# Kernel optimization log

Measured on AMD Instinct MI355X. Metric: run time of the kernel, lower is better.

Reference implementation:

```python
import jax, jax.numpy as jnp
import numpy as np

D = 1024  # input_size
NORM = 1.0 / np.sqrt(D)


def setup_inputs() -> dict:
    key = jax.random.key(0)
    k_x, k_q, k_k, k_v = jax.random.split(key, 4)
    B, S = 4, 2048
    scale = 1.0 / np.sqrt(D)  # init ~ nn.Linear default magnitude
    return {
        "inputs": jax.random.normal(k_x, (B, S, D), dtype=jnp.float32),
        "Wq": jax.random.uniform(k_q, (D, D), jnp.float32, -scale, scale),
        "Wk": jax.random.uniform(k_k, (D, D), jnp.float32, -scale, scale),
        "Wv": jax.random.uniform(k_v, (D, D), jnp.float32, -scale, scale),
    }


def reference(inputs, Wq, Wk, Wv):
    # nn.Linear(x) = x @ W.T (no bias)
    Q = jnp.einsum("bsd,ed->bse", inputs, Wq)
    K = jnp.einsum("bsd,ed->bse", inputs, Wk)
    V = jnp.einsum("bsd,ed->bse", inputs, Wv)
    attn = jnp.einsum("bqe,bke->bqk", Q, K) * NORM  # [B,S,S]
    attn = jax.nn.softmax(attn, axis=2)
    return jnp.einsum("bqk,bke->bqe", attn, V)
```

## Files before the change

kernel.cpp:

```cpp
#include <hip/hip_runtime.h>

typedef __bf16 bf16_t;
typedef __bf16 bf16x8 __attribute__((ext_vector_type(8)));
typedef __bf16 bf16x4 __attribute__((ext_vector_type(4)));
typedef float  floatx4 __attribute__((ext_vector_type(4)));

__device__ __forceinline__ void gload_lds16(const bf16_t* g, bf16_t* l) {
    __builtin_amdgcn_global_load_lds(
        (const __attribute__((address_space(1))) void*)g,
        (__attribute__((address_space(3))) void*)l,
        16, 0, 0);
}

template <int MODE, int BKT, typename OutT>
__global__ __launch_bounds__(256) void gemm_nt(
    const bf16_t* __restrict__ A, int lda, size_t batchA,
    const bf16_t* __restrict__ B, int ldb, size_t batchB,
    OutT* __restrict__ C, int ldc, size_t batchC,
    bf16_t* __restrict__ C2, int ldc2,
    float* __restrict__ rowsums, int batchR,
    int K, float scale)
{
    constexpr int CH  = BKT / 8;
    constexpr int RPS = 2048 / BKT;
    constexpr int NSHOT = 128 / RPS;

    __shared__ bf16_t sA[128 * BKT];
    __shared__ bf16_t sB[128 * BKT];

    A += (size_t)blockIdx.z * batchA;
    B += (size_t)blockIdx.z * batchB;

    const int tid  = threadIdx.x;
    const int wid  = tid >> 6;
    const int lane = tid & 63;

    const int bm = blockIdx.x * 128;
    const int bn = blockIdx.y * 128;

    const int rr  = tid / CH;
    const int kc8 = (((tid & (CH - 1)) ^ (rr & (CH - 1))) << 3);

    const int wy = (wid >> 1) * 64;
    const int wx = (wid & 1) * 64;
    const int lr = lane & 15;

    floatx4 acc[4][4] = {};

    const bf16_t* pa = A + (size_t)(bm + rr) * lda + kc8;
    const bf16_t* pb = B + (size_t)(bn + rr) * ldb + kc8;
    bf16_t* la = &sA[wid * 512];
    bf16_t* lb = &sB[wid * 512];

    for (int k0 = 0; k0 < K; k0 += BKT) {
        #pragma unroll
        for (int c = 0; c < NSHOT; ++c) {
            gload_lds16(pa + (size_t)(c * RPS) * lda + k0, la + c * 2048);
            gload_lds16(pb + (size_t)(c * RPS) * ldb + k0, lb + c * 2048);
        }
        __syncthreads();

        #pragma unroll
        for (int kk = 0; kk < BKT / 32; ++kk) {
            const int cch = (kk << 2) + (lane >> 4);
            bf16x8 af[4], bq[4];
            #pragma unroll
            for (int i = 0; i < 4; ++i) {
                int r = wy + i * 16 + lr;
                af[i] = *(const bf16x8*)&sA[r * BKT + ((cch ^ (r & (CH - 1))) << 3)];
            }
            #pragma unroll
            for (int j = 0; j < 4; ++j) {
                int r = wx + j * 16 + lr;
                bq[j] = *(const bf16x8*)&sB[r * BKT + ((cch ^ (r & (CH - 1))) << 3)];
            }
            #pragma unroll
            for (int i = 0; i < 4; ++i)
                #pragma unroll
                for (int j = 0; j < 4; ++j)
                    acc[i][j] = __builtin_amdgcn_mfma_f32_16x16x32_bf16(
                        bq[j], af[i], acc[i][j], 0, 0, 0);
        }
        __syncthreads();
    }

    const int cfix = lane & 15;
    const int creg = (lane >> 4) << 2;

    if constexpr (MODE == 1) {
        if (blockIdx.z == 2) {
            #pragma unroll
            for (int i = 0; i < 4; ++i) {
                int mg = bm + wy + i * 16 + cfix;
                #pragma unroll
                for (int j = 0; j < 4; ++j) {
                    int ng = bn + wx + j * 16 + creg;
                    #pragma unroll
                    for (int r = 0; r < 4; ++r)
                        C2[(size_t)(ng + r) * ldc2 + mg] = (bf16_t)acc[i][j][r];
                }
            }
            return;
        }
        OutT* Cz = C + (size_t)blockIdx.z * batchC;
        #pragma unroll
        for (int i = 0; i < 4; ++i) {
            size_t row = (size_t)(bm + wy + i * 16 + cfix);
            #pragma unroll
            for (int j = 0; j < 4; ++j) {
                int col = bn + wx + j * 16 + creg;
                bf16x4 v;
                #pragma unroll
                for (int r = 0; r < 4; ++r) v[r] = (bf16_t)acc[i][j][r];
                *(bf16x4*)&Cz[row * (size_t)ldc + col] = v;
            }
        }
    } else if constexpr (MODE == 2) {
        OutT* Cz = C + (size_t)blockIdx.z * batchC;
        float* sums = rowsums + (size_t)blockIdx.z * batchR;
        float rs[4] = {0.f, 0.f, 0.f, 0.f};
        #pragma unroll
        for (int i = 0; i < 4; ++i) {
            size_t row = (size_t)(bm + wy + i * 16 + cfix);
            #pragma unroll
            for (int j = 0; j < 4; ++j) {
                int col = bn + wx + j * 16 + creg;
                bf16x4 v;
                #pragma unroll
                for (int r = 0; r < 4; ++r) {
                    v[r] = (bf16_t)__expf(acc[i][j][r] * scale);
                    rs[i] += (float)v[r];
                }
                *(bf16x4*)&Cz[row * (size_t)ldc + col] = v;
            }
        }
        #pragma unroll
        for (int i = 0; i < 4; ++i) {
            rs[i] += __shfl_xor(rs[i], 16);
            rs[i] += __shfl_xor(rs[i], 32);
        }
        if (lane < 16) {
            #pragma unroll
            for (int i = 0; i < 4; ++i)
                atomicAdd(&sums[bm + wy + i * 16 + lane], rs[i]);
        }
    } else {
        OutT* Cz = C + (size_t)blockIdx.z * batchC;
        const float* sums = rowsums + (size_t)blockIdx.z * batchR;
        #pragma unroll
        for (int i = 0; i < 4; ++i) {
            int rloc = bm + wy + i * 16 + cfix;
            float rinv = 1.0f / sums[rloc];
            size_t row = (size_t)rloc;
            #pragma unroll
            for (int j = 0; j < 4; ++j) {
                int col = bn + wx + j * 16 + creg;
                floatx4 v;
                #pragma unroll
                for (int r = 0; r < 4; ++r) v[r] = acc[i][j][r] * rinv;
                *(floatx4*)&Cz[row * (size_t)ldc + col] = v;
            }
        }
    }
}

__global__ __launch_bounds__(256) void cvt_all(
    const float* __restrict__ X, const float* __restrict__ Wq,
    const float* __restrict__ Wk, const float* __restrict__ Wv,
    bf16_t* __restrict__ Xb, bf16_t* __restrict__ Wqb,
    bf16_t* __restrict__ Wkb, bf16_t* __restrict__ Wvb,
    int nX4, int nW4)
{
    int i = blockIdx.x * blockDim.x + threadIdx.x;
    const float* src; bf16_t* dst; int idx;
    if (i < nX4) { src = X; dst = Xb; idx = i; }
    else {
        int j = i - nX4;
        int w = j / nW4;
        idx = j - w * nW4;
        if (i >= nX4 + 3 * nW4) return;
        src = (w == 0) ? Wq : (w == 1) ? Wk : Wv;
        dst = (w == 0) ? Wqb : (w == 1) ? Wkb : Wvb;
    }
    float4 v = ((const float4*)src)[idx];
    bf16x4 o;
    o[0] = (bf16_t)v.x; o[1] = (bf16_t)v.y; o[2] = (bf16_t)v.z; o[3] = (bf16_t)v.w;
    *(bf16x4*)(dst + (size_t)idx * 4) = o;
}

extern "C" void kernel_launch(void* const* d_in, const int* in_sizes, int n_in,
                              void* d_out, int out_size, void* d_ws, size_t ws_size,
                              hipStream_t stream)
{
    (void)in_sizes; (void)n_in; (void)out_size; (void)ws_size;
    const float* X  = (const float*)d_in[0];
    const float* Wq = (const float*)d_in[1];
    const float* Wk = (const float*)d_in[2];
    const float* Wv = (const float*)d_in[3];
    float* out = (float*)d_out;

    const int Bb = 4, S = 2048, D = 1024;
    const int M = Bb * S;

    char* ws = (char*)d_ws;
    size_t off = 0;
    auto carve = [&](size_t bytes) -> char* {
        char* p = ws + off;
        off += (bytes + 255) & ~(size_t)255;
        return p;
    };
    bf16_t* Xb  = (bf16_t*)carve((size_t)M * D * 2);
    bf16_t* Wqb = (bf16_t*)carve((size_t)D * D * 2);
    bf16_t* Wkb = (bf16_t*)carve((size_t)D * D * 2);
    bf16_t* Wvb = (bf16_t*)carve((size_t)D * D * 2);
    bf16_t* Qb  = (bf16_t*)carve((size_t)M * D * 2);
    bf16_t* Kb  = (bf16_t*)carve((size_t)M * D * 2);
    bf16_t* Vt  = (bf16_t*)carve((size_t)D * M * 2);
    bf16_t* Sc  = (bf16_t*)carve((size_t)Bb * S * S * 2);
    float*  sums = (float*)carve((size_t)M * 4);

    hipMemsetAsync(sums, 0, (size_t)M * 4, stream);

    const int nX4 = M * D / 4, nW4 = D * D / 4;
    const int tot4 = nX4 + 3 * nW4;
    cvt_all<<<(tot4 + 255) / 256, 256, 0, stream>>>(
        X, Wq, Wk, Wv, Xb, Wqb, Wkb, Wvb, nX4, nW4);

    gemm_nt<1, 64, bf16_t><<<dim3(M / 128, D / 128, 3), 256, 0, stream>>>(
        Xb, D, 0, Wqb, D, (size_t)D * D, Qb, D, (size_t)M * D,
        Vt, M, nullptr, 0, D, 1.0f);

    gemm_nt<2, 64, bf16_t><<<dim3(S / 128, S / 128, Bb), 256, 0, stream>>>(
        Qb, D, (size_t)S * D, Kb, D, (size_t)S * D, Sc, S, (size_t)S * S,
        nullptr, 0, sums, S, D, 0.03125f);

    gemm_nt<3, 128, float><<<dim3(S / 128, D / 128, Bb), 256, 0, stream>>>(
        Sc, S, (size_t)S * S, Vt, M, (size_t)S, out, D, (size_t)S * D,
        nullptr, 0, sums, S, S, 1.0f);
}
```

Baseline: 242.9 us.

## Fuse conversion and three GEMM stages into one persistent kernel with grid barriers

Replaces the memset, conversion kernel and three separate GEMM launches with a single persistent 512-block kernel. Stages are separated by atomic-counter grid barriers, and the row-sum zeroing moves into the kernel. The aim is to remove launch overhead and inter-kernel gaps. The cost is a fixed grid of 512 blocks, which reduces parallelism for the QK stage (two tiles per block) and the PV stage, and makes correctness depend on every block being co-resident, with a risk of deadlock if they are not. The PV stage also drops from a 128-wide K tile to 64.

Measured after the change: 407.0 us. 1.68x slower.

```diff
diff --git a/kernel.cpp b/kernel.cpp
--- a/kernel.cpp
+++ b/kernel.cpp
@@ -4,6 +4,21 @@
 typedef __bf16 bf16x8 __attribute__((ext_vector_type(8)));
 typedef __bf16 bf16x4 __attribute__((ext_vector_type(4)));
 typedef float  floatx4 __attribute__((ext_vector_type(4)));
+
+#define BK 64
+#define GRID 512
+#define NTHR 256
+
+__device__ __forceinline__ void grid_barrier(unsigned int* cnt, unsigned int target) {
+    __syncthreads();
+    if (threadIdx.x == 0) {
+        __threadfence();
+        atomicAdd(cnt, 1u);
+        while (atomicAdd(cnt, 0u) < target) __builtin_amdgcn_s_sleep(2);
+        __threadfence();
+    }
+    __syncthreads();
+}
 
 __device__ __forceinline__ void gload_lds16(const bf16_t* g, bf16_t* l) {
     __builtin_amdgcn_global_load_lds(
@@ -12,34 +27,21 @@
         16, 0, 0);
 }
 
-template <int MODE, int BKT, typename OutT>
-__global__ __launch_bounds__(256) void gemm_nt(
-    const bf16_t* __restrict__ A, int lda, size_t batchA,
-    const bf16_t* __restrict__ B, int ldb, size_t batchB,
-    OutT* __restrict__ C, int ldc, size_t batchC,
-    bf16_t* __restrict__ C2, int ldc2,
-    float* __restrict__ rowsums, int batchR,
-    int K, float scale)
+template <int MODE>
+__device__ __forceinline__ void gemm_tile(
+    const bf16_t* __restrict__ A, int lda,
+    const bf16_t* __restrict__ B, int ldb,
+    void* __restrict__ Cv, int ldc,
+    float* __restrict__ sums,
+    int bm, int bn, int K, float scale,
+    bf16_t* sA, bf16_t* sB)
 {
-    constexpr int CH  = BKT / 8;
-    constexpr int RPS = 2048 / BKT;
-    constexpr int NSHOT = 128 / RPS;
-
-    __shared__ bf16_t sA[128 * BKT];
-    __shared__ bf16_t sB[128 * BKT];
-
-    A += (size_t)blockIdx.z * batchA;
-    B += (size_t)blockIdx.z * batchB;
-
     const int tid  = threadIdx.x;
     const int wid  = tid >> 6;
     const int lane = tid & 63;
 
-    const int bm = blockIdx.x * 128;
-    const int bn = blockIdx.y * 128;
-
-    const int rr  = tid / CH;
-    const int kc8 = (((tid & (CH - 1)) ^ (rr & (CH - 1))) << 3);
+    const int rr  = tid >> 3;
+    const int kc8 = (((tid & 7) ^ (rr & 7)) << 3);
 
     const int wy = (wid >> 1) * 64;
     const int wx = (wid & 1) * 64;
@@ -52,27 +54,27 @@
     bf16_t* la = &sA[wid * 512];
     bf16_t* lb = &sB[wid * 512];
 
-    for (int k0 = 0; k0 < K; k0 += BKT) {
-        #pragma unroll
-        for (int c = 0; c < NSHOT; ++c) {
-            gload_lds16(pa + (size_t)(c * RPS) * lda + k0, la + c * 2048);
-            gload_lds16(pb + (size_t)(c * RPS) * ldb + k0, lb + c * 2048);
+    for (int k0 = 0; k0 < K; k0 += BK) {
+        #pragma unroll
+        for (int c = 0; c < 4; ++c) {
+            gload_lds16(pa + (size_t)(c * 32) * lda + k0, la + c * 2048);
+            gload_lds16(pb + (size_t)(c * 32) * ldb + k0, lb + c * 2048);
         }
         __syncthreads();
 
         #pragma unroll
-        for (int kk = 0; kk < BKT / 32; ++kk) {
+        for (int kk = 0; kk < 2; ++kk) {
             const int cch = (kk << 2) + (lane >> 4);
             bf16x8 af[4], bq[4];
             #pragma unroll
             for (int i = 0; i < 4; ++i) {
                 int r = wy + i * 16 + lr;
-                af[i] = *(const bf16x8*)&sA[r * BKT + ((cch ^ (r & (CH - 1))) << 3)];
+                af[i] = *(const bf16x8*)&sA[(r << 6) + ((cch ^ (r & 7)) << 3)];
             }
             #pragma unroll
             for (int j = 0; j < 4; ++j) {
                 int r = wx + j * 16 + lr;
-                bq[j] = *(const bf16x8*)&sB[r * BKT + ((cch ^ (r & (CH - 1))) << 3)];
+                bq[j] = *(const bf16x8*)&sB[(r << 6) + ((cch ^ (r & 7)) << 3)];
             }
             #pragma unroll
             for (int i = 0; i < 4; ++i)
@@ -87,51 +89,47 @@
     const int cfix = lane & 15;
     const int creg = (lane >> 4) << 2;
 
-    if constexpr (MODE == 1) {
-        if (blockIdx.z == 2) {
-            #pragma unroll
-            for (int i = 0; i < 4; ++i) {
-                int mg = bm + wy + i * 16 + cfix;
-                #pragma unroll
-                for (int j = 0; j < 4; ++j) {
-                    int ng = bn + wx + j * 16 + creg;
-                    #pragma unroll
-                    for (int r = 0; r < 4; ++r)
-                        C2[(size_t)(ng + r) * ldc2 + mg] = (bf16_t)acc[i][j][r];
-                }
-            }
-            return;
-        }
-        OutT* Cz = C + (size_t)blockIdx.z * batchC;
+    if constexpr (MODE == 0) {
+        bf16_t* C = (bf16_t*)Cv;
         #pragma unroll
         for (int i = 0; i < 4; ++i) {
             size_t row = (size_t)(bm + wy + i * 16 + cfix);
             #pragma unroll
             for (int j = 0; j < 4; ++j) {
-                int col = bn + wx + j * 16 + creg;
                 bf16x4 v;
                 #pragma unroll
                 for (int r = 0; r < 4; ++r) v[r] = (bf16_t)acc[i][j][r];
-                *(bf16x4*)&Cz[row * (size_t)ldc + col] = v;
+                *(bf16x4*)&C[row * (size_t)ldc + (bn + wx + j * 16 + creg)] = v;
+            }
+        }
+    } else if constexpr (MODE == 4) {
+        bf16_t* C = (bf16_t*)Cv;
+        #pragma unroll
+        for (int i = 0; i < 4; ++i) {
+            int mg = bm + wy + i * 16 + cfix;
+            #pragma unroll
+            for (int j = 0; j < 4; ++j) {
+                int ng = bn + wx + j * 16 + creg;
+                #pragma unroll
+                for (int r = 0; r < 4; ++r)
+                    C[(size_t)(ng + r) * ldc + mg] = (bf16_t)acc[i][j][r];
             }
         }
     } else if constexpr (MODE == 2) {
-        OutT* Cz = C + (size_t)blockIdx.z * batchC;
-        float* sums = rowsums + (size_t)blockIdx.z * batchR;
+        bf16_t* C = (bf16_t*)Cv;
         float rs[4] = {0.f, 0.f, 0.f, 0.f};
         #pragma unroll
         for (int i = 0; i < 4; ++i) {
             size_t row = (size_t)(bm + wy + i * 16 + cfix);
             #pragma unroll
             for (int j = 0; j < 4; ++j) {
-                int col = bn + wx + j * 16 + creg;
                 bf16x4 v;
                 #pragma unroll
                 for (int r = 0; r < 4; ++r) {
                     v[r] = (bf16_t)__expf(acc[i][j][r] * scale);
                     rs[i] += (float)v[r];
                 }
-                *(bf16x4*)&Cz[row * (size_t)ldc + col] = v;
+                *(bf16x4*)&C[row * (size_t)ldc + (bn + wx + j * 16 + creg)] = v;
             }
         }
         #pragma unroll
@@ -145,47 +143,95 @@
                 atomicAdd(&sums[bm + wy + i * 16 + lane], rs[i]);
         }
     } else {
-        OutT* Cz = C + (size_t)blockIdx.z * batchC;
-        const float* sums = rowsums + (size_t)blockIdx.z * batchR;
+        float* C = (float*)Cv;
         #pragma unroll
         for (int i = 0; i < 4; ++i) {
             int rloc = bm + wy + i * 16 + cfix;
             float rinv = 1.0f / sums[rloc];
-            size_t row = (size_t)rloc;
-            #pragma unroll
-            for (int j = 0; j < 4; ++j) {
-                int col = bn + wx + j * 16 + creg;
+            #pragma unroll
+            for (int j = 0; j < 4; ++j) {
                 floatx4 v;
                 #pragma unroll
                 for (int r = 0; r < 4; ++r) v[r] = acc[i][j][r] * rinv;
-                *(floatx4*)&Cz[row * (size_t)ldc + col] = v;
-            }
-        }
-    }
-}
-
-__global__ __launch_bounds__(256) void cvt_all(
-    const float* __restrict__ X, const float* __restrict__ Wq,
-    const float* __restrict__ Wk, const float* __restrict__ Wv,
-    bf16_t* __restrict__ Xb, bf16_t* __restrict__ Wqb,
-    bf16_t* __restrict__ Wkb, bf16_t* __restrict__ Wvb,
-    int nX4, int nW4)
+                *(floatx4*)&C[(size_t)rloc * ldc + (bn + wx + j * 16 + creg)] = v;
+            }
+        }
+    }
+}
+
+struct Params {
+    const float *X, *Wq, *Wk, *Wv;
+    bf16_t *Xb, *Wqb, *Wkb, *Wvb, *Qb, *Kb, *Vt, *Sc;
+    float* sums;
+    float* out;
+    unsigned int* cnt;
+};
+
+__global__ __launch_bounds__(NTHR, 2) void attn_mega(Params p)
 {
-    int i = blockIdx.x * blockDim.x + threadIdx.x;
-    const float* src; bf16_t* dst; int idx;
-    if (i < nX4) { src = X; dst = Xb; idx = i; }
-    else {
-        int j = i - nX4;
-        int w = j / nW4;
-        idx = j - w * nW4;
-        if (i >= nX4 + 3 * nW4) return;
-        src = (w == 0) ? Wq : (w == 1) ? Wk : Wv;
-        dst = (w == 0) ? Wqb : (w == 1) ? Wkb : Wvb;
-    }
-    float4 v = ((const float4*)src)[idx];
-    bf16x4 o;
-    o[0] = (bf16_t)v.x; o[1] = (bf16_t)v.y; o[2] = (bf16_t)v.z; o[3] = (bf16_t)v.w;
-    *(bf16x4*)(dst + (size_t)idx * 4) = o;
+    constexpr int S = 2048, D = 1024, M = 8192;
+    constexpr int nX4 = M * D / 4;
+    constexpr int nW4 = D * D / 4;
+    constexpr int tot4 = nX4 + 3 * nW4;
+
+    __shared__ bf16_t sA[128 * BK];
+    __shared__ bf16_t sB[128 * BK];
+
+    const int tid = threadIdx.x;
+    const int blk = blockIdx.x;
+
+    for (int i = blk * NTHR + tid; i < tot4; i += GRID * NTHR) {
+        const float* src; bf16_t* dst; int idx;
+        if (i < nX4) { src = p.X; dst = p.Xb; idx = i; }
+        else {
+            int j = i - nX4;
+            int w = j >> 18;
+            idx = j & (nW4 - 1);
+            src = (w == 0) ? p.Wq : (w == 1) ? p.Wk : p.Wv;
+            dst = (w == 0) ? p.Wqb : (w == 1) ? p.Wkb : p.Wvb;
+        }
+        float4 v = ((const float4*)src)[idx];
+        bf16x4 o;
+        o[0] = (bf16_t)v.x; o[1] = (bf16_t)v.y; o[2] = (bf16_t)v.z; o[3] = (bf16_t)v.w;
+        *(bf16x4*)(dst + (size_t)idx * 4) = o;
+    }
+    {
+        int gi = blk * NTHR + tid;
+        if (gi < M) p.sums[gi] = 0.f;
+    }
+    grid_barrier(p.cnt, GRID);
+
+    {
+        const int bm = (blk & 63) * 128;
+        const int bn = (blk >> 6) * 128;
+        gemm_tile<0>(p.Xb, D, p.Wqb, D, p.Qb, D, nullptr, bm, bn, D, 1.0f, sA, sB);
+        gemm_tile<0>(p.Xb, D, p.Wkb, D, p.Kb, D, nullptr, bm, bn, D, 1.0f, sA, sB);
+        gemm_tile<4>(p.Xb, D, p.Wvb, D, p.Vt, M, nullptr, bm, bn, D, 1.0f, sA, sB);
+    }
+    grid_barrier(p.cnt, 2 * GRID);
+
+    #pragma unroll
+    for (int half = 0; half < 2; ++half) {
+        int t = blk + half * GRID;
+        int z   = t >> 8;
+        int rem = t & 255;
+        int bm = (rem & 15) * 128, bn = (rem >> 4) * 128;
+        gemm_tile<2>(p.Qb + (size_t)z * S * D, D,
+                     p.Kb + (size_t)z * S * D, D,
+                     p.Sc + (size_t)z * S * S, S,
+                     p.sums + z * S, bm, bn, D, 0.03125f, sA, sB);
+    }
+    grid_barrier(p.cnt, 3 * GRID);
+
+    {
+        int z   = blk >> 7;
+        int rem = blk & 127;
+        int bm = (rem & 15) * 128, bn = (rem >> 4) * 128;
+        gemm_tile<3>(p.Sc + (size_t)z * S * S, S,
+                     p.Vt + (size_t)z * S, M,
+                     p.out + (size_t)z * S * D, D,
+                     p.sums + z * S, bm, bn, S, 1.0f, sA, sB);
+    }
 }
 
 extern "C" void kernel_launch(void* const* d_in, const int* in_sizes, int n_in,
@@ -193,48 +239,35 @@
                               hipStream_t stream)
 {
     (void)in_sizes; (void)n_in; (void)out_size; (void)ws_size;
-    const float* X  = (const float*)d_in[0];
-    const float* Wq = (const float*)d_in[1];
-    const float* Wk = (const float*)d_in[2];
-    const float* Wv = (const float*)d_in[3];
-    float* out = (float*)d_out;
-
     const int Bb = 4, S = 2048, D = 1024;
     const int M = Bb * S;
 
     char* ws = (char*)d_ws;
     size_t off = 0;
     auto carve = [&](size_t bytes) -> char* {
-        char* p = ws + off;
+        char* pp = ws + off;
         off += (bytes + 255) & ~(size_t)255;
-        return p;
+        return pp;
     };
-    bf16_t* Xb  = (bf16_t*)carve((size_t)M * D * 2);
-    bf16_t* Wqb = (bf16_t*)carve((size_t)D * D * 2);
-    bf16_t* Wkb = (bf16_t*)carve((size_t)D * D * 2);
-    bf16_t* Wvb = (bf16_t*)carve((size_t)D * D * 2);
-    bf16_t* Qb  = (bf16_t*)carve((size_t)M * D * 2);
-    bf16_t* Kb  = (bf16_t*)carve((size_t)M * D * 2);
-    bf16_t* Vt  = (bf16_t*)carve((size_t)D * M * 2);
-    bf16_t* Sc  = (bf16_t*)carve((size_t)Bb * S * S * 2);
-    float*  sums = (float*)carve((size_t)M * 4);
-
-    hipMemsetAsync(sums, 0, (size_t)M * 4, stream);
-
-    const int nX4 = M * D / 4, nW4 = D * D / 4;
-    const int tot4 = nX4 + 3 * nW4;
-    cvt_all<<<(tot4 + 255) / 256, 256, 0, stream>>>(
-        X, Wq, Wk, Wv, Xb, Wqb, Wkb, Wvb, nX4, nW4);
-
-    gemm_nt<1, 64, bf16_t><<<dim3(M / 128, D / 128, 3), 256, 0, stream>>>(
-        Xb, D, 0, Wqb, D, (size_t)D * D, Qb, D, (size_t)M * D,
-        Vt, M, nullptr, 0, D, 1.0f);
-
-    gemm_nt<2, 64, bf16_t><<<dim3(S / 128, S / 128, Bb), 256, 0, stream>>>(
-        Qb, D, (size_t)S * D, Kb, D, (size_t)S * D, Sc, S, (size_t)S * S,
-        nullptr, 0, sums, S, D, 0.03125f);
-
-    gemm_nt<3, 128, float><<<dim3(S / 128, D / 128, Bb), 256, 0, stream>>>(
-        Sc, S, (size_t)S * S, Vt, M, (size_t)S, out, D, (size_t)S * D,
-        nullptr, 0, sums, S, S, 1.0f);
-}
+
+    Params p;
+    p.X  = (const float*)d_in[0];
+    p.Wq = (const float*)d_in[1];
+    p.Wk = (const float*)d_in[2];
+    p.Wv = (const float*)d_in[3];
+    p.out = (float*)d_out;
+    p.Xb  = (bf16_t*)carve((size_t)M * D * 2);
+    p.Wqb = (bf16_t*)carve((size_t)D * D * 2);
+    p.Wkb = (bf16_t*)carve((size_t)D * D * 2);
+    p.Wvb = (bf16_t*)carve((size_t)D * D * 2);
+    p.Qb  = (bf16_t*)carve((size_t)M * D * 2);
+    p.Kb  = (bf16_t*)carve((size_t)M * D * 2);
+    p.Vt  = (bf16_t*)carve((size_t)D * M * 2);
+    p.Sc  = (bf16_t*)carve((size_t)Bb * S * S * 2);
+    p.sums = (float*)carve((size_t)M * 4);
+    p.cnt  = (unsigned int*)carve(256);
+
+    hipMemsetAsync(p.cnt, 0, sizeof(unsigned int), stream);
+
+    attn_mega<<<GRID, NTHR, 0, stream>>>(p);
+}
```
